# Performance work log

Measured on AMD Instinct MI355X. Metric: run time of the kernel, lower is better.

## Reference

```python
import jax, jax.numpy as jnp
import numpy as np

D_MODEL = 1024
N_HEADS = 16
N_MEM = 64
D_K = D_MODEL // N_HEADS


def setup_inputs() -> dict:
    key = jax.random.key(0)
    ks = jax.random.split(key, 16)
    B, N = 2, 2048
    s = 1.0 / np.sqrt(D_MODEL)  # xavier-ish scale
    inp = {
        "q": jax.random.normal(ks[0], (B, N, D_MODEL), jnp.float32),
        "k": jax.random.normal(ks[1], (B, N, D_MODEL), jnp.float32),
        "v": jax.random.normal(ks[2], (B, N, D_MODEL), jnp.float32),
        "attention_mask": jax.random.randint(ks[3], (B, 1, 1, N), 0, 2).astype(bool),
        "Wq": jax.random.normal(ks[4], (D_MODEL, D_MODEL), jnp.float32) * s,
        "bq": jnp.zeros((D_MODEL,), jnp.float32),
        "Wk": jax.random.normal(ks[5], (D_MODEL, D_MODEL), jnp.float32) * s,
        "bk": jnp.zeros((D_MODEL,), jnp.float32),
        "Wv": jax.random.normal(ks[6], (D_MODEL, D_MODEL), jnp.float32) * s,
        "bv": jnp.zeros((D_MODEL,), jnp.float32),
        "Wo": jax.random.normal(ks[7], (D_MODEL, D_MODEL), jnp.float32) * s,
        "bo": jnp.zeros((D_MODEL,), jnp.float32),
        "m_k": jax.random.normal(ks[8], (1, N_MEM, D_MODEL), jnp.float32) * 0.01,
        "m_v": jax.random.normal(ks[9], (1, N_MEM, D_MODEL), jnp.float32) * 0.01,
    }
    return inp


def reference(q, k, v, attention_mask, Wq, bq, Wk, bk, Wv, bv, Wo, bo, m_k, m_v):
    B, Nq, D = q.shape
    nk = k.shape[1]
    H, dk, M = N_HEADS, D_K, N_MEM

    # projections (torch Linear: x @ W.T + b)
    qh = (q @ Wq.T + bq).reshape(B, Nq, H, dk).transpose(0, 2, 1, 3)  # b h nq d
    k_proj = k @ Wk.T + bk                                            # b nk d_model
    v_proj = v @ Wv.T + bv

    # append scaled memory slots along key/value length
    mk = jnp.broadcast_to(m_k * np.sqrt(dk), (B, M, D))
    mv = jnp.broadcast_to(m_v * np.sqrt(M), (B, M, D))
    kk = jnp.concatenate([k_proj, mk], axis=1)                        # b (nk+M) d_model
    vv = jnp.concatenate([v_proj, mv], axis=1)

    kh = kk.reshape(B, nk + M, H, dk).transpose(0, 2, 1, 3)          # b h nkM d
    vh = vv.reshape(B, nk + M, H, dk).transpose(0, 2, 1, 3)

    scores = jnp.einsum('bhqd,bhkd->bhqk', qh, kh) / np.sqrt(dk)      # b h nq (nk+M)

    # mask applies only to the first nk key positions; memory slots unmasked
    pad_mask = jnp.concatenate(
        [jnp.broadcast_to(attention_mask, (B, 1, 1, nk)),
         jnp.zeros((B, 1, 1, M), bool)], axis=-1)
    scores = jnp.where(pad_mask, -jnp.inf, scores)

    p_attn = jax.nn.softmax(scores, axis=-1)  # dropout p=0.0 -> identity
    out = jnp.einsum('bhqk,bhkd->bhqd', p_attn, vh)
    out = out.transpose(0, 2, 1, 3).reshape(B, Nq, D)
    return out @ Wo.T + bo
```

## Files before the change

kernel.cpp:

```cpp
#include <hip/hip_runtime.h>
#include <hip/hip_bf16.h>

typedef __attribute__((ext_vector_type(8))) short bf16x8;
typedef __attribute__((ext_vector_type(4))) float f32x4;

__device__ __forceinline__ short f2b(float x) {
    __hip_bfloat16 h = __float2bfloat16(x);
    short s;
    __builtin_memcpy(&s, &h, 2);
    return s;
}

__device__ __forceinline__ void gload16(const short* g, const short* l) {
    __builtin_amdgcn_global_load_lds((const __attribute__((address_space(1))) void*)g,
                                     (__attribute__((address_space(3))) void*)l, 16, 0, 0);
}

__global__ __launch_bounds__(256) void k_prep(const float* __restrict__ q,
                                              const float* __restrict__ k,
                                              const float* __restrict__ v,
                                              const float* __restrict__ Wq,
                                              const float* __restrict__ Wk,
                                              const float* __restrict__ Wv,
                                              const float* __restrict__ Wo,
                                              const float* __restrict__ mk,
                                              const float* __restrict__ mv,
                                              short* __restrict__ dst,
                                              short* __restrict__ kcat,
                                              short* __restrict__ vcat,
                                              short* __restrict__ vt) {
    const int y = blockIdx.y;
    const int i0 = blockIdx.x * 256 + threadIdx.x;
    if (y < 3) {
        const float* src = (y == 0) ? q : (y == 1) ? k : v;
        size_t base = (size_t)y * 1048576;
        #pragma unroll
        for (int it = 0; it < 4; ++it) {
            int off = i0 + it * 262144;
            float4 val = ((const float4*)src)[off];
            short4 o;
            o.x = f2b(val.x); o.y = f2b(val.y); o.z = f2b(val.z); o.w = f2b(val.w);
            ((short4*)dst)[base + off] = o;
        }
    } else if (y < 7) {
        const float* src = (y == 3) ? Wq : (y == 4) ? Wk : (y == 5) ? Wv : Wo;
        size_t base = 3145728 + (size_t)(y - 3) * 262144;
        float4 val = ((const float4*)src)[i0];
        short4 o;
        o.x = f2b(val.x); o.y = f2b(val.y); o.z = f2b(val.z); o.w = f2b(val.w);
        ((short4*)dst)[base + i0] = o;
    } else {
        if (i0 < 131072) {
            int b = i0 >> 16;
            int r = (i0 >> 10) & 63;
            int d = i0 & 1023;
            kcat[((size_t)(b * 2176 + 2048 + r)) * 1024 + d] = f2b(mk[r * 1024 + d] * 8.0f);
            vcat[((size_t)(b * 2176 + 2048 + r)) * 1024 + d] = f2b(mv[r * 1024 + d] * 8.0f);
            kcat[((size_t)(b * 2176 + 2112 + r)) * 1024 + d] = 0;
            int h = (i0 >> 12) & 15, dd = (i0 >> 6) & 63, c = i0 & 63;
            vt[((size_t)((b * 16 + h) * 64 + dd)) * 2176 + 2112 + c] = 0;
        }
    }
}

template <int MODE>
__device__ __forceinline__ void gemm_core(const short* __restrict__ A,
                                          const short* __restrict__ Bw,
                                          const float* __restrict__ bias,
                                          void* __restrict__ Cout,
                                          int bm, int bn,
                                          short (*As)[32], short (*Bs)[32]) {
    const int tid = threadIdx.x;
    const int w = tid >> 6, lane = tid & 63;
    const int wm = w >> 1, wn = w & 1;
    const int lr = lane & 15, lg = lane >> 4;
    const int rseg = lane >> 2;
    const int c_src = (lane & 3) ^ ((lane >> 3) & 3);
    const int slot = lg ^ ((lr >> 1) & 3);

    const short* Ab = A + (size_t)(bm * 128) * 1024;
    const short* Bb = Bw + (size_t)(bn * 128) * 1024;

    f32x4 acc[4][4] = {};

    for (int k0 = 0; k0 < 1024; k0 += 32) {
        __syncthreads();
        #pragma unroll
        for (int jj = 0; jj < 2; ++jj) {
            int seg = w * 2 + jj;
            int row = seg * 16 + rseg;
            gload16(Ab + (size_t)row * 1024 + k0 + c_src * 8, &As[seg * 16][0]);
            gload16(Bb + (size_t)row * 1024 + k0 + c_src * 8, &Bs[seg * 16][0]);
        }
        __syncthreads();
        bf16x8 af[4], bfr[4];
        #pragma unroll
        for (int m = 0; m < 4; ++m) {
            int row = wm * 64 + m * 16 + lr;
            af[m] = *(const bf16x8*)((const char*)As + row * 64 + slot * 16);
        }
        #pragma unroll
        for (int n = 0; n < 4; ++n) {
            int row = wn * 64 + n * 16 + lr;
            bfr[n] = *(const bf16x8*)((const char*)Bs + row * 64 + slot * 16);
        }
        #pragma unroll
        for (int m = 0; m < 4; ++m)
            #pragma unroll
            for (int n = 0; n < 4; ++n)
                acc[m][n] = __builtin_amdgcn_mfma_f32_16x16x32_bf16(af[m], bfr[n], acc[m][n], 0, 0, 0);
    }

    #pragma unroll
    for (int m = 0; m < 4; ++m) {
        #pragma unroll
        for (int n = 0; n < 4; ++n) {
            int col = bn * 128 + wn * 64 + n * 16 + lr;
            float bv = bias[col];
            #pragma unroll
            for (int r = 0; r < 4; ++r) {
                int row = bm * 128 + wm * 64 + m * 16 + lg * 4 + r;
                float val = acc[m][n][r] + bv;
                if (MODE == 0) {
                    ((short*)Cout)[(size_t)row * 1024 + col] = f2b(val);
                } else if (MODE == 1) {
                    int rr = (row >> 11) * 2176 + (row & 2047);
                    ((short*)Cout)[(size_t)rr * 1024 + col] = f2b(val);
                } else {
                    ((float*)Cout)[(size_t)row * 1024 + col] = val;
                }
            }
        }
    }
}

__global__ __launch_bounds__(256) void k_gemm_qkv(const short* __restrict__ qb,
                                                  const short* __restrict__ kb,
                                                  const short* __restrict__ vb,
                                                  const short* __restrict__ Wqb,
                                                  const short* __restrict__ Wkb,
                                                  const short* __restrict__ Wvb,
                                                  const float* __restrict__ bq,
                                                  const float* __restrict__ bk,
                                                  const float* __restrict__ bv,
                                                  short* __restrict__ qp,
                                                  short* __restrict__ kcat,
                                                  short* __restrict__ vcat) {
    __shared__ __align__(16) short As[128][32];
    __shared__ __align__(16) short Bs[128][32];
    const int z = blockIdx.z;
    if (z == 0)      gemm_core<0>(qb, Wqb, bq, qp,   blockIdx.x, blockIdx.y, As, Bs);
    else if (z == 1) gemm_core<1>(kb, Wkb, bk, kcat, blockIdx.x, blockIdx.y, As, Bs);
    else             gemm_core<1>(vb, Wvb, bv, vcat, blockIdx.x, blockIdx.y, As, Bs);
}

__global__ __launch_bounds__(256) void k_gemm_o(const short* __restrict__ aout,
                                                const short* __restrict__ Wob,
                                                const float* __restrict__ bo,
                                                float* __restrict__ out) {
    __shared__ __align__(16) short As[128][32];
    __shared__ __align__(16) short Bs[128][32];
    gemm_core<2>(aout, Wob, bo, out, blockIdx.x, blockIdx.y, As, Bs);
}

__global__ __launch_bounds__(256) void k_vtrans(const short* __restrict__ vcat,
                                                short* __restrict__ vt) {
    __shared__ __align__(16) short t[64][72];
    const int kk0 = blockIdx.x * 64, h = blockIdx.y, b = blockIdx.z;
    const int tid = threadIdx.x;
    const int r = tid >> 3, c = tid & 7;
    #pragma unroll
    for (int i = 0; i < 2; ++i) {
        int row = r + i * 32;
        bf16x8 v = *(const bf16x8*)(vcat + ((size_t)(b * 2176 + kk0 + row)) * 1024 + h * 64 + c * 8);
        *(bf16x8*)(&t[row][c * 8]) = v;
    }
    __syncthreads();
    #pragma unroll
    for (int i = 0; i < 2; ++i) {
        int d = r + i * 32;
        bf16x8 outv;
        #pragma unroll
        for (int j = 0; j < 8; ++j) outv[j] = t[c * 8 + j][d];
        *(bf16x8*)(vt + ((size_t)((b * 16 + h) * 64 + d)) * 2176 + kk0 + c * 8) = outv;
    }
}

__global__ __launch_bounds__(512) void k_attn(const short* __restrict__ qp,
                                              const short* __restrict__ kcat,
                                              const short* __restrict__ vt,
                                              const int* __restrict__ maskI,
                                              short* __restrict__ aout) {
    __shared__ __align__(16) short Ks[2][64][64];
    __shared__ __align__(16) short Vs[2][64][64];
    __shared__ __align__(16) short Pt[8][16][72];
    __shared__ float smask[2176];

    const int bid = blockIdx.x;
    const int x = bid & 7, j = bid >> 3;
    const int g = x + 8 * (j & 3);
    const int qt = j >> 2;
    const int h = g & 15, b = g >> 4;

    const int tid = threadIdx.x;
    const int w = tid >> 6, lane = tid & 63;
    const int lr = lane & 15, lg = lane >> 4;

    for (int i = tid; i < 2176; i += 512) {
        float mval;
        if (i < 2048) mval = maskI[b * 2048 + i] ? -INFINITY : 0.0f;
        else          mval = 0.0f;
        smask[i] = mval;
    }

    const short* Kb = kcat + (size_t)b * 2176 * 1024 + h * 64;
    const short* Vb = vt + ((size_t)(b * 16 + h) * 64) * 2176;

    const int srow8 = lane >> 3;
    const int schunk = (lane & 7) ^ srow8;

    {
        int row = w * 8 + srow8;
        gload16(Kb + (size_t)row * 1024 + schunk * 8, &Ks[0][w * 8][0]);
        gload16(Vb + (size_t)row * 2176 + schunk * 8, &Vs[0][w * 8][0]);
    }

    const size_t qbase = ((size_t)(b * 2048 + qt * 128 + w * 16)) * 1024 + h * 64;
    bf16x8 qf[2];
    #pragma unroll
    for (int ks = 0; ks < 2; ++ks)
        qf[ks] = *(const bf16x8*)(qp + qbase + (size_t)lr * 1024 + ks * 32 + lg * 8);

    float m_run = -1e30f, l_part = 0.0f;
    f32x4 o[4] = {};

    __syncthreads();

    int cur = 0;
    for (int t = 0; t < 33; ++t) {
        const int key0 = t * 64;

        if (t < 32) {
            const int nk0 = key0 + 64;
            int row = w * 8 + srow8;
            gload16(Kb + (size_t)(nk0 + row) * 1024 + schunk * 8, &Ks[cur ^ 1][w * 8][0]);
            gload16(Vb + (size_t)row * 2176 + nk0 + schunk * 8, &Vs[cur ^ 1][w * 8][0]);
        }

        f32x4 s[4] = {};
        #pragma unroll
        for (int ks = 0; ks < 2; ++ks)
            #pragma unroll
            for (int n = 0; n < 4; ++n) {
                int krow = n * 16 + lr;
                int kchunk = (ks * 4 + lg) ^ (lr & 7);
                bf16x8 kf = *(const bf16x8*)((const char*)(&Ks[cur][0][0]) + krow * 128 + kchunk * 16);
                s[n] = __builtin_amdgcn_mfma_f32_16x16x32_bf16(kf, qf[ks], s[n], 0, 0, 0);
            }

        float lm = -1e30f;
        #pragma unroll
        for (int n = 0; n < 4; ++n) {
            float4 mq = *(const float4*)(&smask[key0 + n * 16 + lg * 4]);
            s[n][0] = s[n][0] * 0.125f + mq.x;
            s[n][1] = s[n][1] * 0.125f + mq.y;
            s[n][2] = s[n][2] * 0.125f + mq.z;
            s[n][3] = s[n][3] * 0.125f + mq.w;
            lm = fmaxf(lm, fmaxf(fmaxf(s[n][0], s[n][1]), fmaxf(s[n][2], s[n][3])));
        }

        if (__any(lm - m_run > 3.0f)) {
            float tm = lm;
            tm = fmaxf(tm, __shfl_xor(tm, 16));
            tm = fmaxf(tm, __shfl_xor(tm, 32));
            float mnew = fmaxf(m_run, tm);
            float corr = __expf(m_run - mnew);
            m_run = mnew;
            l_part *= corr;
            #pragma unroll
            for (int r = 0; r < 4; ++r) {
                float cb = __shfl(corr, 20 * lg + r);
                #pragma unroll
                for (int nO = 0; nO < 4; ++nO) o[nO][r] *= cb;
            }
        }

        #pragma unroll
        for (int n = 0; n < 4; ++n) {
            float p0 = __expf(s[n][0] - m_run);
            float p1 = __expf(s[n][1] - m_run);
            float p2 = __expf(s[n][2] - m_run);
            float p3 = __expf(s[n][3] - m_run);
            l_part += (p0 + p1) + (p2 + p3);
            unsigned pk[2];
            pk[0] = (unsigned)(unsigned short)f2b(p0) | ((unsigned)(unsigned short)f2b(p1) << 16);
            pk[1] = (unsigned)(unsigned short)f2b(p2) | ((unsigned)(unsigned short)f2b(p3) << 16);
            __builtin_memcpy((char*)(&Pt[w][0][0]) + lr * 144 + n * 32 + lg * 8, pk, 8);
        }

        asm volatile("s_waitcnt lgkmcnt(0)" ::: "memory");
        __builtin_amdgcn_sched_barrier(0);

        #pragma unroll
        for (int ks2 = 0; ks2 < 2; ++ks2) {
            bf16x8 pa;
            __builtin_memcpy(&pa, (const char*)(&Pt[w][0][0]) + lr * 144 + ks2 * 64 + lg * 16, 16);
            #pragma unroll
            for (int nO = 0; nO < 4; ++nO) {
                int vrow = nO * 16 + lr;
                int vchunk = (ks2 * 4 + lg) ^ (lr & 7);
                bf16x8 vf = *(const bf16x8*)((const char*)(&Vs[cur][0][0]) + vrow * 128 + vchunk * 16);
                o[nO] = __builtin_amdgcn_mfma_f32_16x16x32_bf16(pa, vf, o[nO], 0, 0, 0);
            }
        }

        __syncthreads();
        cur ^= 1;
    }

    float l = l_part;
    l += __shfl_xor(l, 16);
    l += __shfl_xor(l, 32);
    float inv = 1.0f / l;
    #pragma unroll
    for (int r = 0; r < 4; ++r) {
        float ib = __shfl(inv, 20 * lg + r);
        int qrow = qt * 128 + w * 16 + lg * 4 + r;
        #pragma unroll
        for (int nO = 0; nO < 4; ++nO)
            aout[((size_t)(b * 2048 + qrow)) * 1024 + h * 64 + nO * 16 + lr] =
                f2b(o[nO][r] * ib);
    }
}

extern "C" void kernel_launch(void* const* d_in, const int* in_sizes, int n_in,
                              void* d_out, int out_size, void* d_ws, size_t ws_size,
                              hipStream_t stream) {
    const float* q  = (const float*)d_in[0];
    const float* k  = (const float*)d_in[1];
    const float* v  = (const float*)d_in[2];
    const int* mask = (const int*)d_in[3];
    const float* Wq = (const float*)d_in[4];
    const float* bq = (const float*)d_in[5];
    const float* Wk = (const float*)d_in[6];
    const float* bk = (const float*)d_in[7];
    const float* Wv = (const float*)d_in[8];
    const float* bv = (const float*)d_in[9];
    const float* Wo = (const float*)d_in[10];
    const float* bo = (const float*)d_in[11];
    const float* mk = (const float*)d_in[12];
    const float* mv = (const float*)d_in[13];

    char* ws = (char*)d_ws;
    size_t off = 0;
    auto alloc = [&](size_t bytes) {
        char* p = ws + off;
        off += (bytes + 255) & ~(size_t)255;
        return p;
    };
    short* qb   = (short*)alloc(4096ull * 1024 * 2);
    short* kb   = (short*)alloc(4096ull * 1024 * 2);
    short* vb   = (short*)alloc(4096ull * 1024 * 2);
    short* Wqb  = (short*)alloc(1024ull * 1024 * 2);
    short* Wkb  = (short*)alloc(1024ull * 1024 * 2);
    short* Wvb  = (short*)alloc(1024ull * 1024 * 2);
    short* Wob  = (short*)alloc(1024ull * 1024 * 2);
    short* qp   = (short*)alloc(4096ull * 1024 * 2);
    short* kcat = (short*)alloc(2ull * 2176 * 1024 * 2);
    short* vcat = (short*)alloc(2ull * 2176 * 1024 * 2);
    short* vtb  = (short*)alloc(2ull * 16 * 64 * 2176 * 2);
    short* aout = (short*)alloc(4096ull * 1024 * 2);

    k_prep<<<dim3(1024, 8), 256, 0, stream>>>(q, k, v, Wq, Wk, Wv, Wo, mk, mv,
                                              qb, kcat, vcat, vtb);

    k_gemm_qkv<<<dim3(32, 8, 3), 256, 0, stream>>>(qb, kb, vb, Wqb, Wkb, Wvb,
                                                   bq, bk, bv, qp, kcat, vcat);

    k_vtrans<<<dim3(33, 16, 2), 256, 0, stream>>>(vcat, vtb);

    k_attn<<<512, 512, 0, stream>>>(qp, kcat, vtb, mask, aout);

    k_gemm_o<<<dim3(32, 8), 256, 0, stream>>>(aout, Wob, bo, (float*)d_out);
}
```

Before: 141.4 us.

## Feed softmax probabilities directly from registers into 16x16x16 MFMA for PV

Removes the per-wave LDS staging buffer for P. The S accumulator layout already matches the A operand of the 16x16x16 bf16 MFMA, so P is packed in registers and fed directly, with V read in 4-element chunks from the swizzled tile. This drops an LDS write, a waitcnt and an LDS read per tile, at the cost of twice as many (smaller) MFMAs and narrower V loads. It also folds log2(e) into the score scale so exp2 replaces expf, and raises the lazy rescale threshold.

```diff
diff --git a/kernel.cpp b/kernel.cpp
--- a/kernel.cpp
+++ b/kernel.cpp
@@ -2,6 +2,7 @@
 #include <hip/hip_bf16.h>
 
 typedef __attribute__((ext_vector_type(8))) short bf16x8;
+typedef __attribute__((ext_vector_type(4))) short bf16x4;
 typedef __attribute__((ext_vector_type(4))) float f32x4;
 
 __device__ __forceinline__ short f2b(float x) {
@@ -14,6 +15,19 @@
 __device__ __forceinline__ void gload16(const short* g, const short* l) {
     __builtin_amdgcn_global_load_lds((const __attribute__((address_space(1))) void*)g,
                                      (__attribute__((address_space(3))) void*)l, 16, 0, 0);
+}
+
+__device__ __forceinline__ f32x4 mfma16(bf16x4 a, bf16x4 b, f32x4 c) {
+#if __has_builtin(__builtin_amdgcn_mfma_f32_16x16x16bf16_1k)
+    return __builtin_amdgcn_mfma_f32_16x16x16bf16_1k(a, b, c, 0, 0, 0);
+#else
+    asm volatile("s_nop 1\n\t"
+                 "v_mfma_f32_16x16x16_bf16 %0, %1, %2, %0\n\t"
+                 "s_nop 7\n\t"
+                 "s_nop 3"
+                 : "+v"(c) : "v"(a), "v"(b));
+    return c;
+#endif
 }
 
 __global__ __launch_bounds__(256) void k_prep(const float* __restrict__ q,
@@ -193,7 +207,6 @@
                                               short* __restrict__ aout) {
     __shared__ __align__(16) short Ks[2][64][64];
     __shared__ __align__(16) short Vs[2][64][64];
-    __shared__ __align__(16) short Pt[8][16][72];
     __shared__ float smask[2176];
 
     const int bid = blockIdx.x;
@@ -231,6 +244,7 @@
     for (int ks = 0; ks < 2; ++ks)
         qf[ks] = *(const bf16x8*)(qp + qbase + (size_t)lr * 1024 + ks * 32 + lg * 8);
 
+    const float C2 = 0.18033688011f;
     float m_run = -1e30f, l_part = 0.0f;
     f32x4 o[4] = {};
 
@@ -262,19 +276,19 @@
         #pragma unroll
         for (int n = 0; n < 4; ++n) {
             float4 mq = *(const float4*)(&smask[key0 + n * 16 + lg * 4]);
-            s[n][0] = s[n][0] * 0.125f + mq.x;
-            s[n][1] = s[n][1] * 0.125f + mq.y;
-            s[n][2] = s[n][2] * 0.125f + mq.z;
-            s[n][3] = s[n][3] * 0.125f + mq.w;
+            s[n][0] = fmaf(s[n][0], C2, mq.x);
+            s[n][1] = fmaf(s[n][1], C2, mq.y);
+            s[n][2] = fmaf(s[n][2], C2, mq.z);
+            s[n][3] = fmaf(s[n][3], C2, mq.w);
             lm = fmaxf(lm, fmaxf(fmaxf(s[n][0], s[n][1]), fmaxf(s[n][2], s[n][3])));
         }
 
-        if (__any(lm - m_run > 3.0f)) {
+        if (__any(lm - m_run > 4.0f)) {
             float tm = lm;
             tm = fmaxf(tm, __shfl_xor(tm, 16));
             tm = fmaxf(tm, __shfl_xor(tm, 32));
             float mnew = fmaxf(m_run, tm);
-            float corr = __expf(m_run - mnew);
+            float corr = exp2f(m_run - mnew);
             m_run = mnew;
             l_part *= corr;
             #pragma unroll
@@ -285,32 +299,28 @@
             }
         }
 
+        bf16x4 pa16[4];
         #pragma unroll
         for (int n = 0; n < 4; ++n) {
-            float p0 = __expf(s[n][0] - m_run);
-            float p1 = __expf(s[n][1] - m_run);
-            float p2 = __expf(s[n][2] - m_run);
-            float p3 = __expf(s[n][3] - m_run);
+            float p0 = exp2f(s[n][0] - m_run);
+            float p1 = exp2f(s[n][1] - m_run);
+            float p2 = exp2f(s[n][2] - m_run);
+            float p3 = exp2f(s[n][3] - m_run);
             l_part += (p0 + p1) + (p2 + p3);
-            unsigned pk[2];
-            pk[0] = (unsigned)(unsigned short)f2b(p0) | ((unsigned)(unsigned short)f2b(p1) << 16);
-            pk[1] = (unsigned)(unsigned short)f2b(p2) | ((unsigned)(unsigned short)f2b(p3) << 16);
-            __builtin_memcpy((char*)(&Pt[w][0][0]) + lr * 144 + n * 32 + lg * 8, pk, 8);
-        }
-
-        asm volatile("s_waitcnt lgkmcnt(0)" ::: "memory");
-        __builtin_amdgcn_sched_barrier(0);
-
-        #pragma unroll
-        for (int ks2 = 0; ks2 < 2; ++ks2) {
-            bf16x8 pa;
-            __builtin_memcpy(&pa, (const char*)(&Pt[w][0][0]) + lr * 144 + ks2 * 64 + lg * 16, 16);
+            bf16x4 pa;
+            pa[0] = f2b(p0); pa[1] = f2b(p1); pa[2] = f2b(p2); pa[3] = f2b(p3);
+            pa16[n] = pa;
+        }
+
+        #pragma unroll
+        for (int kb = 0; kb < 4; ++kb) {
             #pragma unroll
             for (int nO = 0; nO < 4; ++nO) {
                 int vrow = nO * 16 + lr;
-                int vchunk = (ks2 * 4 + lg) ^ (lr & 7);
-                bf16x8 vf = *(const bf16x8*)((const char*)(&Vs[cur][0][0]) + vrow * 128 + vchunk * 16);
-                o[nO] = __builtin_amdgcn_mfma_f32_16x16x32_bf16(pa, vf, o[nO], 0, 0, 0);
+                int e8 = kb * 4 + lg;
+                int boff = vrow * 128 + (((e8 >> 1) ^ (lr & 7)) << 4) + ((e8 & 1) << 3);
+                bf16x4 vf = *(const bf16x4*)((const char*)(&Vs[cur][0][0]) + boff);
+                o[nO] = mfma16(pa16[kb], vf, o[nO]);
             }
         }
 
```

Result: slower. 154.5 us (+9.3%).
